# Optimization experiments

Measured on AMD Instinct MI355X. Metric: run time of the kernel, lower is better.

Reference implementation:

```python
import jax, jax.numpy as jnp
import numpy as np

N, TI, TO1 = 8, 200, 51
V, E, H, J, L = 1024, 512, 512, 512, 3
ENC_D = 512


def setup_inputs() -> dict:
    key = jax.random.key(0)
    ks = jax.random.split(key, 11)
    s = lambda k, shape, sc: jax.random.normal(k, shape, jnp.float32) * sc
    return {
        "enc_out": s(ks[0], (N, TI, ENC_D), 1.0),
        "tgt_pad": jax.random.randint(ks[1], (N, TO1), 0, V),
        "embed": s(ks[2], (V, E), 0.02),          # nn.Embedding weight
        "w_ih": s(ks[3], (L, 4 * H, E), 0.04),    # LSTM input-hidden (gate order i,f,g,o)
        "w_hh": s(ks[4], (L, 4 * H, H), 0.04),    # LSTM hidden-hidden
        "b_ih": s(ks[5], (L, 4 * H), 0.04),
        "b_hh": s(ks[6], (L, 4 * H), 0.04),
        "enc_w": s(ks[7], (J, ENC_D), 0.04),      # enc_proj (no bias)
        "dec_w": s(ks[8], (J, H), 0.04),          # dec_proj weight
        "dec_b": s(ks[9], (J,), 0.04),            # dec_proj bias
        "out_w": s(ks[10], (V, J), 0.04),         # output (no bias)
    }


def lstm_layer(x, wih, whh, bih, bhh):
    # x: [N, T, E] -> [N, T, H]; PyTorch LSTM gate order i, f, g, o
    n = x.shape[0]
    h0 = jnp.zeros((n, whh.shape[1]), x.dtype)
    c0 = jnp.zeros_like(h0)
    gin = jnp.einsum('nte,ge->ntg', x, wih) + bih + bhh  # precompute input contributions

    def step(carry, g_t):
        h, c = carry
        g = g_t + h @ whh.T
        i, f, gg, o = jnp.split(g, 4, axis=-1)
        c = jax.nn.sigmoid(f) * c + jax.nn.sigmoid(i) * jnp.tanh(gg)
        h = jax.nn.sigmoid(o) * jnp.tanh(c)
        return (h, c), h

    _, hs = jax.lax.scan(step, (h0, c0), jnp.swapaxes(gin, 0, 1))
    return jnp.swapaxes(hs, 0, 1)


def reference(enc_out, tgt_pad, embed, w_ih, w_hh, b_ih, b_hh, enc_w, dec_w, dec_b, out_w):
    # embedding lookup
    x = embed[tgt_pad]                                   # [N, To+1, E]
    # 3-layer unidirectional LSTM
    for l in range(w_ih.shape[0]):
        x = lstm_layer(x, w_ih[l], w_hh[l], b_ih[l], b_hh[l])
    # projections
    enc_p = jnp.einsum('ntd,jd->ntj', enc_out, enc_w)    # [N, Ti, J]
    dec_p = jnp.einsum('nud,jd->nuj', x, dec_w) + dec_b  # [N, To+1, J]
    # joint: broadcast add -> tanh -> output linear (no bias)
    add = enc_p[:, :, None, :] + dec_p[:, None, :, :]    # [N, Ti, To+1, J]
    return jnp.einsum('ntuj,vj->ntuv', jnp.tanh(add), out_w)  # [N, Ti, To+1, V]
```

## Files before the change

### kernel.cpp

```cpp
#include <hip/hip_runtime.h>
#include <cstdint>
#include <cstddef>

typedef __attribute__((ext_vector_type(4))) float f32x4;
typedef __attribute__((ext_vector_type(8))) short bf16x8;
typedef __attribute__((ext_vector_type(8))) unsigned short u16x8;
typedef __attribute__((ext_vector_type(4))) float float4v;
typedef __attribute__((ext_vector_type(2))) unsigned long long u64x2;
typedef unsigned long long ull;

#define NB   8
#define TIN  200
#define TO1  51
#define VSZ  1024
#define HSZ  512
static constexpr int MJOINT = NB * TIN * TO1;
static constexpr int MROWS  = TO1 * NB;

static constexpr size_t B_ENCBF = 0;
static constexpr size_t B_ENCW  = B_ENCBF + 1664ull*512*2;
static constexpr size_t B_DECW  = B_ENCW  + 512ull*512*2;
static constexpr size_t B_OUTW  = B_DECW  + 512ull*512*2;
static constexpr size_t B_WIH   = B_OUTW  + 1024ull*512*2;
static constexpr size_t B_WHH   = B_WIH   + 3ull*2048*512*2;
static constexpr size_t B_XTR   = B_WHH   + 3ull*2048*512*2;
static constexpr size_t B_BSUM  = B_XTR   + 4ull*408*512*2;
static constexpr size_t B_FLAGS = B_BSUM  + 3ull*2048*4;
static constexpr size_t B_ENCP  = B_FLAGS + 8192;
static constexpr size_t B_DECP  = B_ENCP  + 1664ull*512*4;
static constexpr size_t B_ABUF  = B_DECP  + 512ull*512*4;

__device__ __forceinline__ unsigned short f2bf(float f) {
  union { float f; unsigned u; } v; v.f = f;
  unsigned r = v.u + 0x7FFFu + ((v.u >> 16) & 1u);
  return (unsigned short)(r >> 16);
}
__device__ __forceinline__ float fast_tanh(float x) {
  float t = __expf(2.0f * x);
  return 1.0f - 2.0f / (t + 1.0f);
}
__device__ __forceinline__ float fast_sig(float x) {
  return 1.0f / (1.0f + __expf(-x));
}
__device__ __forceinline__ void gll16(const void* g, void* l) {
  __builtin_amdgcn_global_load_lds(
      (const __attribute__((address_space(1))) unsigned int*)g,
      (__attribute__((address_space(3))) unsigned int*)l, 16, 0, 0);
}
__device__ __forceinline__ void cvt8(const float* s, unsigned short* d) {
  const float4v* sp = (const float4v*)s;
  float4v x = sp[0], y = sp[1];
  u16x8 o;
  o[0]=f2bf(x[0]); o[1]=f2bf(x[1]); o[2]=f2bf(x[2]); o[3]=f2bf(x[3]);
  o[4]=f2bf(y[0]); o[5]=f2bf(y[1]); o[6]=f2bf(y[2]); o[7]=f2bf(y[3]);
  *(u16x8*)d = o;
}

static constexpr int N_ENC  = 102400;
static constexpr int N_ENCW = 32768;
static constexpr int N_DECW = 32768;
static constexpr int N_OUTW = 65536;
static constexpr int N_WIH  = 393216;
static constexpr int P0 = N_ENC, P1 = P0+N_ENCW, P2 = P1+N_DECW, P3 = P2+N_OUTW,
                     P4 = P3+N_WIH;

__global__ __launch_bounds__(256) void cvt_all(const float* __restrict__ enc,
                                               const float* __restrict__ encw,
                                               const float* __restrict__ decw,
                                               const float* __restrict__ outw,
                                               const float* __restrict__ wih,
                                               const float* __restrict__ whh,
                                               unsigned short* __restrict__ d_enc,
                                               unsigned short* __restrict__ d_encw,
                                               unsigned short* __restrict__ d_decw,
                                               unsigned short* __restrict__ d_outw,
                                               unsigned short* __restrict__ d_wih,
                                               unsigned short* __restrict__ d_whh) {
  int i = blockIdx.x * 256 + threadIdx.x;
  const float* s; unsigned short* d; int rel;
  if      (i < P0) { s = enc;  d = d_enc;  rel = i; }
  else if (i < P1) { s = encw; d = d_encw; rel = i - P0; }
  else if (i < P2) { s = decw; d = d_decw; rel = i - P1; }
  else if (i < P3) { s = outw; d = d_outw; rel = i - P2; }
  else if (i < P4) { s = wih;  d = d_wih;  rel = i - P3; }
  else             { s = whh;  d = d_whh;  rel = i - P4; }
  cvt8(s + (size_t)rel * 8, d + (size_t)rel * 8);
}

__global__ __launch_bounds__(256) void bsum_kernel(const float* __restrict__ a,
                                                   const float* __restrict__ b,
                                                   float* __restrict__ o, int n) {
  int i = blockIdx.x * 256 + threadIdx.x;
  if (i < n) o[i] = a[i] + b[i];
}

__global__ __launch_bounds__(256) void embed_kernel(const float* __restrict__ emb,
                                                    const int* __restrict__ tgt,
                                                    unsigned short* __restrict__ x0) {
  int idx = blockIdx.x * 256 + threadIdx.x;
  if (idx >= MROWS * 64) return;
  int m = idx >> 6, kc = (idx & 63) * 8;
  int t = m >> 3, n = m & 7;
  int v = tgt[n * TO1 + t];
  cvt8(emb + (size_t)v * 512 + kc, x0 + (size_t)m * 512 + kc);
}

__global__ __launch_bounds__(256) void gemm_bf16(const unsigned short* __restrict__ A,
                                                 const unsigned short* __restrict__ B,
                                                 float* __restrict__ C,
                                                 const float* __restrict__ bias,
                                                 int M, int N, int K) {
  __shared__ __align__(16) unsigned short lds[2][2][4096];
  const int tid = threadIdx.x;
  const int wave = tid >> 6, lane = tid & 63;
  const int lr = lane & 15, lg = lane >> 4;
  const int wm = (wave >> 1) * 64, wn = (wave & 1) * 64;
  const int xsl = (lg ^ (lr & 3)) << 3;

  const int nwg = gridDim.x * gridDim.y;
  const int id = blockIdx.y * gridDim.x + blockIdx.x;
  const int q = nwg >> 3, r = nwg & 7, xcd = id & 7, rest = id >> 3;
  const int nid = (xcd < r ? xcd * (q + 1) : r * (q + 1) + (xcd - r) * q) + rest;
  const size_t n0 = (size_t)(nid % gridDim.x) * 128;
  const size_t m0 = (size_t)(nid / gridDim.x) * 128;

  f32x4 acc[4][4];
#pragma unroll
  for (int i = 0; i < 4; ++i)
#pragma unroll
    for (int j = 0; j < 4; ++j) acc[i][j] = (f32x4){0.f, 0.f, 0.f, 0.f};

#define STAGE(bf, kt)                                                                 \
  do {                                                                                \
    _Pragma("unroll") for (int u = 0; u < 2; ++u) {                                   \
      const int s = u * 256 + tid;                                                    \
      const int row_ = s >> 2;                                                        \
      const int ch = (s & 3) ^ (row_ & 3);                                            \
      gll16(A + (m0 + row_) * (size_t)K + (kt) + ch * 8,                              \
            &lds[bf][0][(u * 256 + wave * 64) * 8]);                                  \
    }                                                                                 \
    _Pragma("unroll") for (int u = 0; u < 2; ++u) {                                   \
      const int s = u * 256 + tid;                                                    \
      const int row_ = s >> 2;                                                        \
      const int ch = (s & 3) ^ (row_ & 3);                                            \
      gll16(B + (n0 + row_) * (size_t)K + (kt) + ch * 8,                              \
            &lds[bf][1][(u * 256 + wave * 64) * 8]);                                  \
    }                                                                                 \
  } while (0)

  const int nt = K >> 5;
  int cur = 0;
  STAGE(0, 0);
  for (int t = 0; t < nt; ++t) {
    if (t + 1 < nt) {
      STAGE(cur ^ 1, (t + 1) * 32);
      asm volatile("s_waitcnt vmcnt(4)" ::: "memory");
    } else {
      asm volatile("s_waitcnt vmcnt(0)" ::: "memory");
    }
    __builtin_amdgcn_s_barrier();
    const unsigned short* As_ = lds[cur][0];
    const unsigned short* Bs_ = lds[cur][1];
    bf16x8 a[4], b[4];
#pragma unroll
    for (int i = 0; i < 4; ++i) a[i] = *(const bf16x8*)&As_[(wm + i * 16 + lr) * 32 + xsl];
#pragma unroll
    for (int j = 0; j < 4; ++j) b[j] = *(const bf16x8*)&Bs_[(wn + j * 16 + lr) * 32 + xsl];
    __builtin_amdgcn_s_setprio(1);
#pragma unroll
    for (int i = 0; i < 4; ++i)
#pragma unroll
      for (int j = 0; j < 4; ++j)
        acc[i][j] = __builtin_amdgcn_mfma_f32_16x16x32_bf16(a[i], b[j], acc[i][j], 0, 0, 0);
    __builtin_amdgcn_s_setprio(0);
    __builtin_amdgcn_s_barrier();
    cur ^= 1;
  }
#undef STAGE

  const int rq = lg * 4;
#pragma unroll
  for (int j = 0; j < 4; ++j) {
    const int col = (int)n0 + wn + j * 16 + lr;
    const float bv = bias ? bias[col] : 0.0f;
#pragma unroll
    for (int i = 0; i < 4; ++i) {
#pragma unroll
      for (int q2 = 0; q2 < 4; ++q2) {
        const long m = (long)m0 + wm + i * 16 + rq + q2;
        if (m < M) C[(size_t)m * N + col] = acc[i][j][q2] + bv;
      }
    }
  }
}

__global__ __launch_bounds__(512, 2) void gemm256(const unsigned short* __restrict__ A,
                                                  const unsigned short* __restrict__ B,
                                                  float* __restrict__ C,
                                                  int M, int N, int K) {
  __shared__ __align__(16) unsigned short lds[2][2][16384];
  const int tid = threadIdx.x;
  const int wave = tid >> 6, lane = tid & 63;
  const int lr = lane & 15, lg = lane >> 4;
  const int wr = (wave >> 2) * 128;
  const int wc = (wave & 3) * 64;

  const int nwg = gridDim.x * gridDim.y;
  const int id = blockIdx.y * gridDim.x + blockIdx.x;
  const int q = nwg >> 3, r = nwg & 7, xcd = id & 7, rest = id >> 3;
  const int nid = (xcd < r ? xcd * (q + 1) : r * (q + 1) + (xcd - r) * q) + rest;
  const size_t n0 = (size_t)(nid % gridDim.x) * 256;
  const size_t m0 = (size_t)(nid / gridDim.x) * 256;

  f32x4 acc[8][4];
#pragma unroll
  for (int i = 0; i < 8; ++i)
#pragma unroll
    for (int j = 0; j < 4; ++j) acc[i][j] = (f32x4){0.f, 0.f, 0.f, 0.f};

#define STG(bf, kt)                                                                    \
  do {                                                                                 \
    _Pragma("unroll") for (int u = 0; u < 4; ++u) {                                    \
      const int idx = u * 512 + tid;                                                   \
      const int row_ = idx >> 3;                                                       \
      const int ch = (idx & 7) ^ (row_ & 7);                                           \
      gll16(A + (m0 + row_) * (size_t)K + (kt) + ch * 8,                               \
            &lds[bf][0][(u * 512 + wave * 64) * 8]);                                   \
    }                                                                                  \
    _Pragma("unroll") for (int u = 0; u < 4; ++u) {                                    \
      const int idx = u * 512 + tid;                                                   \
      const int row_ = idx >> 3;                                                       \
      const int ch = (idx & 7) ^ (row_ & 7);                                           \
      gll16(B + (n0 + row_) * (size_t)K + (kt) + ch * 8,                               \
            &lds[bf][1][(u * 512 + wave * 64) * 8]);                                   \
    }                                                                                  \
  } while (0)

  const int nt = K >> 6;
  int cur = 0;
  STG(0, 0);
  for (int t = 0; t < nt; ++t) {
    if (t + 1 < nt) {
      STG(cur ^ 1, (t + 1) * 64);
      asm volatile("s_waitcnt vmcnt(8)" ::: "memory");
    } else {
      asm volatile("s_waitcnt vmcnt(0)" ::: "memory");
    }
    __builtin_amdgcn_s_barrier();
    const unsigned short* As_ = lds[cur][0];
    const unsigned short* Bs_ = lds[cur][1];
    bf16x8 b[4][2];
#pragma unroll
    for (int j = 0; j < 4; ++j) {
      const int rb = wc + j * 16 + lr;
      const int sw = rb & 7;
      b[j][0] = *(const bf16x8*)&Bs_[rb * 64 + ((lg ^ sw) << 3)];
      b[j][1] = *(const bf16x8*)&Bs_[rb * 64 + (((4 + lg) ^ sw) << 3)];
    }
    __builtin_amdgcn_s_setprio(1);
#pragma unroll
    for (int i = 0; i < 8; ++i) {
      const int ra = wr + i * 16 + lr;
      const int swa = ra & 7;
      bf16x8 a0 = *(const bf16x8*)&As_[ra * 64 + ((lg ^ swa) << 3)];
      bf16x8 a1 = *(const bf16x8*)&As_[ra * 64 + (((4 + lg) ^ swa) << 3)];
#pragma unroll
      for (int j = 0; j < 4; ++j) {
        acc[i][j] = __builtin_amdgcn_mfma_f32_16x16x32_bf16(a0, b[j][0], acc[i][j], 0, 0, 0);
        acc[i][j] = __builtin_amdgcn_mfma_f32_16x16x32_bf16(a1, b[j][1], acc[i][j], 0, 0, 0);
      }
    }
    __builtin_amdgcn_s_setprio(0);
    __builtin_amdgcn_s_barrier();
    cur ^= 1;
  }
#undef STG

#pragma unroll
  for (int i = 0; i < 8; ++i) {
#pragma unroll
    for (int q2 = 0; q2 < 4; ++q2) {
      const long m = (long)m0 + wr + i * 16 + lg * 4 + q2;
      if (m < M) {
        float* crow = C + (size_t)m * N + n0 + wc;
#pragma unroll
        for (int j = 0; j < 4; ++j) crow[j * 16 + lr] = acc[i][j][q2];
      }
    }
  }
}

__global__ __launch_bounds__(256) void rnn_kernel(const unsigned short* __restrict__ wih,
                                                  const unsigned short* __restrict__ whh,
                                                  const float* __restrict__ bsum,
                                                  unsigned short* __restrict__ xtr,
                                                  int* __restrict__ flags) {
  __shared__ __align__(16) unsigned short w_s[64 * 1024];
  __shared__ __align__(16) unsigned short x_s[8 * 512];
  __shared__ __align__(16) unsigned short h_s[8 * 512];
  __shared__ float gates_s[4][8][16];

  const int tid = threadIdx.x;
  const int l = blockIdx.x >> 5;
  const int b32 = blockIdx.x & 31;
  const int hid0 = b32 << 4;
  const int wave = tid >> 6, lane = tid & 63;
  const int lr = lane & 15, lg = lane >> 4;
  const int r7 = lr & 7;
  const int rw = wave * 16 + lr;

  {
    const int rl = tid >> 2;
    const int qt = tid & 3;
    const size_t R = (size_t)l * 2048 + (size_t)(rl >> 4) * 512 + hid0 + (rl & 15);
    const unsigned short* s0 = wih + R * 512;
    const unsigned short* s1 = whh + R * 512;
#pragma unroll
    for (int i = 0; i < 32; ++i) {
      int c = qt * 32 + i;
      bf16x8 wv = (c < 64) ? *(const bf16x8*)&s0[c * 8] : *(const bf16x8*)&s1[(c - 64) * 8];
      *(bf16x8*)&w_s[rl * 1024 + ((c ^ (rl & 7)) << 3)] = wv;
    }
  }
  const float bias = bsum[(size_t)l * 2048 + (size_t)wave * 512 + hid0 + lr];

  const unsigned short* xin = xtr + (size_t)l * MROWS * 512;
  unsigned short* xout = xtr + (size_t)(l + 1) * MROWS * 512;
  float c_reg = 0.f;
  const int srow = tid >> 5;
  const int sc = tid & 31;
  __syncthreads();

#define STAGE_TILE(SRC_ROW0, BUF)                                                      \
  do {                                                                                 \
    const ull* p_ = (const ull*)((SRC_ROW0) + (size_t)srow * 512);                     \
    _Pragma("unroll") for (int k_ = 0; k_ < 2; ++k_) {                                 \
      const int c_ = sc + k_ * 32;                                                     \
      ull v0_ = __hip_atomic_load(p_ + c_ * 2,     __ATOMIC_RELAXED, __HIP_MEMORY_SCOPE_AGENT); \
      ull v1_ = __hip_atomic_load(p_ + c_ * 2 + 1, __ATOMIC_RELAXED, __HIP_MEMORY_SCOPE_AGENT); \
      *(u64x2*)&(BUF)[srow * 512 + ((c_ ^ srow) << 3)] = (u64x2){v0_, v1_};            \
    }                                                                                  \
  } while (0)

#define POLL(FIDX_EXPR, NEED)                                                          \
  do {                                                                                 \
    if (wave == 0) {                                                                   \
      for (;;) {                                                                       \
        bool ok_ = true;                                                               \
        if (lane < 32)                                                                 \
          ok_ = __hip_atomic_load(&flags[(FIDX_EXPR) * 16], __ATOMIC_RELAXED,          \
                                  __HIP_MEMORY_SCOPE_AGENT) >= (NEED);                 \
        if (__all(ok_)) break;                                                         \
        __builtin_amdgcn_s_sleep(1);                                                   \
      }                                                                                \
    }                                                                                  \
  } while (0)

  f32x4 ax0, ax1;

  if (l > 0) POLL((l - 1) * 32 + lane, 1);
  __syncthreads();
  STAGE_TILE(xin, x_s);
  __syncthreads();
  ax0 = (f32x4){0.f, 0.f, 0.f, 0.f};
  ax1 = (f32x4){0.f, 0.f, 0.f, 0.f};
#pragma unroll
  for (int c16 = 0; c16 < 16; ++c16) {
    const int cc = c16 * 4 + lg;
    bf16x8 av = *(const bf16x8*)&x_s[r7 * 512 + ((cc ^ r7) << 3)];
    bf16x8 bv = *(const bf16x8*)&w_s[rw * 1024 + ((cc ^ r7) << 3)];
    if (c16 & 1) ax1 = __builtin_amdgcn_mfma_f32_16x16x32_bf16(av, bv, ax1, 0, 0, 0);
    else         ax0 = __builtin_amdgcn_mfma_f32_16x16x32_bf16(av, bv, ax0, 0, 0, 0);
  }

  for (int t = 0; t < TO1; ++t) {
    f32x4 acc0 = ax0, acc1 = ax1;
    if (t > 0) {
      POLL(l * 32 + lane, t);
      __syncthreads();
      STAGE_TILE(xout + (size_t)(t - 1) * 8 * 512, h_s);
      __syncthreads();
#pragma unroll
      for (int c16 = 0; c16 < 16; ++c16) {
        const int cc = c16 * 4 + lg;
        bf16x8 av = *(const bf16x8*)&h_s[r7 * 512 + ((cc ^ r7) << 3)];
        bf16x8 bv = *(const bf16x8*)&w_s[rw * 1024 + (((64 + cc) ^ r7) << 3)];
        if (c16 & 1) acc1 = __builtin_amdgcn_mfma_f32_16x16x32_bf16(av, bv, acc1, 0, 0, 0);
        else         acc0 = __builtin_amdgcn_mfma_f32_16x16x32_bf16(av, bv, acc0, 0, 0, 0);
      }
    }

    {
      f32x4 g = acc0 + acc1;
      const int nb4 = lg * 4;
#pragma unroll
      for (int q2 = 0; q2 < 4; ++q2) {
        int n = nb4 + q2;
        if (n < 8) gates_s[wave][n][lr] = g[q2] + bias;
      }
    }
    __syncthreads();
    if (tid < 128) {
      const int n = tid >> 4, j = tid & 15;
      float gi = gates_s[0][n][j], gf = gates_s[1][n][j];
      float gg = gates_s[2][n][j], go = gates_s[3][n][j];
      c_reg = fast_sig(gf) * c_reg + fast_sig(gi) * fast_tanh(gg);
      float ht = fast_sig(go) * fast_tanh(c_reg);
      float htn = __shfl_down(ht, 1);
      if (!(j & 1)) {
        unsigned pk = (unsigned)f2bf(ht) | ((unsigned)f2bf(htn) << 16);
        unsigned* dst = (unsigned*)(xout + ((size_t)t * 8 + n) * 512 + hid0 + j);
        __hip_atomic_store(dst, pk, __ATOMIC_RELAXED, __HIP_MEMORY_SCOPE_AGENT);
      }
    }
    asm volatile("s_waitcnt vmcnt(0)" ::: "memory");
    __syncthreads();
    if (tid == 0)
      __hip_atomic_store(&flags[(l * 32 + b32) * 16], t + 1,
                         __ATOMIC_RELAXED, __HIP_MEMORY_SCOPE_AGENT);

    if (t + 1 < TO1) {
      if (l > 0) POLL((l - 1) * 32 + lane, t + 2);
      __syncthreads();
      STAGE_TILE(xin + (size_t)(t + 1) * 8 * 512, x_s);
      __syncthreads();
      ax0 = (f32x4){0.f, 0.f, 0.f, 0.f};
      ax1 = (f32x4){0.f, 0.f, 0.f, 0.f};
#pragma unroll
      for (int c16 = 0; c16 < 16; ++c16) {
        const int cc = c16 * 4 + lg;
        bf16x8 av = *(const bf16x8*)&x_s[r7 * 512 + ((cc ^ r7) << 3)];
        bf16x8 bv = *(const bf16x8*)&w_s[rw * 1024 + ((cc ^ r7) << 3)];
        if (c16 & 1) ax1 = __builtin_amdgcn_mfma_f32_16x16x32_bf16(av, bv, ax1, 0, 0, 0);
        else         ax0 = __builtin_amdgcn_mfma_f32_16x16x32_bf16(av, bv, ax0, 0, 0, 0);
      }
    }
  }
#undef STAGE_TILE
#undef POLL
}

__global__ __launch_bounds__(256) void tanha_kernel(const float* __restrict__ encp,
                                                    const float* __restrict__ decp,
                                                    unsigned short* __restrict__ Ab) {
  size_t idx = (size_t)blockIdx.x * 256 + threadIdx.x;
  int m = (int)(idx >> 6);
  int kc = ((int)idx & 63) * 8;
  if (m >= 81664) return;
  u16x8 o;
  if (m >= MJOINT) {
    o[0]=0;o[1]=0;o[2]=0;o[3]=0;o[4]=0;o[5]=0;o[6]=0;o[7]=0;
  } else {
    int n = m / (TIN * TO1);
    int rem = m - n * (TIN * TO1);
    int t = rem / TO1;
    int u = rem - t * TO1;
    const float4v* ep = (const float4v*)(encp + ((size_t)n * TIN + t) * 512 + kc);
    const float4v* dp = (const float4v*)(decp + ((size_t)u * 8 + n) * 512 + kc);
    float4v e0 = ep[0], e1 = ep[1], d0 = dp[0], d1 = dp[1];
    o[0]=f2bf(fast_tanh(e0[0]+d0[0])); o[1]=f2bf(fast_tanh(e0[1]+d0[1]));
    o[2]=f2bf(fast_tanh(e0[2]+d0[2])); o[3]=f2bf(fast_tanh(e0[3]+d0[3]));
    o[4]=f2bf(fast_tanh(e1[0]+d1[0])); o[5]=f2bf(fast_tanh(e1[1]+d1[1]));
    o[6]=f2bf(fast_tanh(e1[2]+d1[2])); o[7]=f2bf(fast_tanh(e1[3]+d1[3]));
  }
  *(u16x8*)(Ab + (size_t)m * 512 + kc) = o;
}

extern "C" void kernel_launch(void* const* d_in, const int* in_sizes, int n_in,
                              void* d_out, int out_size, void* d_ws, size_t ws_size,
                              hipStream_t stream) {
  (void)in_sizes; (void)n_in; (void)out_size; (void)ws_size;
  const float* enc_out = (const float*)d_in[0];
  const int*   tgt     = (const int*)d_in[1];
  const float* embed   = (const float*)d_in[2];
  const float* w_ih    = (const float*)d_in[3];
  const float* w_hh    = (const float*)d_in[4];
  const float* b_ih    = (const float*)d_in[5];
  const float* b_hh    = (const float*)d_in[6];
  const float* enc_w   = (const float*)d_in[7];
  const float* dec_w   = (const float*)d_in[8];
  const float* dec_b   = (const float*)d_in[9];
  const float* out_w   = (const float*)d_in[10];

  char* ws = (char*)d_ws;
  unsigned short* enc_bf  = (unsigned short*)(ws + B_ENCBF);
  unsigned short* encw_bf = (unsigned short*)(ws + B_ENCW);
  unsigned short* decw_bf = (unsigned short*)(ws + B_DECW);
  unsigned short* outw_bf = (unsigned short*)(ws + B_OUTW);
  unsigned short* wih_bf  = (unsigned short*)(ws + B_WIH);
  unsigned short* whh_bf  = (unsigned short*)(ws + B_WHH);
  unsigned short* xtr     = (unsigned short*)(ws + B_XTR);
  float* bsum  = (float*)(ws + B_BSUM);
  int*   flags = (int*)(ws + B_FLAGS);
  float* encp  = (float*)(ws + B_ENCP);
  float* decp  = (float*)(ws + B_DECP);
  unsigned short* abuf = (unsigned short*)(ws + B_ABUF);
  float* Cout  = (float*)d_out;

  hipMemsetAsync(flags, 0, 6144, stream);

  cvt_all<<<3984, 256, 0, stream>>>(enc_out, enc_w, dec_w, out_w, w_ih, w_hh,
                                    enc_bf, encw_bf, decw_bf, outw_bf, wih_bf, whh_bf);
  bsum_kernel<<<24, 256, 0, stream>>>(b_ih, b_hh, bsum, 6144);
  embed_kernel<<<102, 256, 0, stream>>>(embed, tgt, xtr);

  rnn_kernel<<<96, 256, 0, stream>>>(wih_bf, whh_bf, bsum, xtr, flags);

  gemm_bf16<<<dim3(4, 13), 256, 0, stream>>>(enc_bf, encw_bf, encp, nullptr, NB * TIN, 512, 512);
  gemm_bf16<<<dim3(4, 4), 256, 0, stream>>>(xtr + 3ull * MROWS * 512, decw_bf, decp, dec_b,
                                            MROWS, 512, 512);
  tanha_kernel<<<20416, 256, 0, stream>>>(encp, decp, abuf);
  gemm256<<<dim3(4, 319), 512, 0, stream>>>(abuf, outw_bf, Cout, MJOINT, VSZ, 512);
}
```

Baseline: 388.5 us.

## Fuse tanh joint into output GEMM A-load and overlap enc projection with RNN

The separate tanh kernel and its 81664x512 bf16 staging buffer are removed. The output GEMM now computes tanh(enc_p+dec_p) in registers and writes it into LDS as its A tile. The encoder projection GEMM runs as 52 extra blocks inside the RNN launch so it overlaps the latency-bound recurrence, and the flag memset moves into the convert kernel. In exchange, each GEMM tile recomputes tanh from fp32 loads with register staging instead of async LDS loads. The 2-waves occupancy hint is dropped, and a full vmcnt(0) wait plus syncthreads per k-step may reduce overlap.

```diff
diff --git a/kernel.cpp b/kernel.cpp
--- a/kernel.cpp
+++ b/kernel.cpp
@@ -28,7 +28,6 @@
 static constexpr size_t B_FLAGS = B_BSUM  + 3ull*2048*4;
 static constexpr size_t B_ENCP  = B_FLAGS + 8192;
 static constexpr size_t B_DECP  = B_ENCP  + 1664ull*512*4;
-static constexpr size_t B_ABUF  = B_DECP  + 512ull*512*4;
 
 __device__ __forceinline__ unsigned short f2bf(float f) {
   union { float f; unsigned u; } v; v.f = f;
@@ -75,7 +74,9 @@
                                                unsigned short* __restrict__ d_decw,
                                                unsigned short* __restrict__ d_outw,
                                                unsigned short* __restrict__ d_wih,
-                                               unsigned short* __restrict__ d_whh) {
+                                               unsigned short* __restrict__ d_whh,
+                                               int* __restrict__ flags) {
+  if (blockIdx.x == 0 && threadIdx.x < 96) flags[threadIdx.x * 16] = 0;
   int i = blockIdx.x * 256 + threadIdx.x;
   const float* s; unsigned short* d; int rel;
   if      (i < P0) { s = enc;  d = d_enc;  rel = i; }
@@ -194,10 +195,10 @@
   }
 }
 
-__global__ __launch_bounds__(512, 2) void gemm256(const unsigned short* __restrict__ A,
-                                                  const unsigned short* __restrict__ B,
-                                                  float* __restrict__ C,
-                                                  int M, int N, int K) {
+__global__ __launch_bounds__(512) void gemm256f(const float* __restrict__ encp,
+                                                const float* __restrict__ decp,
+                                                const unsigned short* __restrict__ B,
+                                                float* __restrict__ C) {
   __shared__ __align__(16) unsigned short lds[2][2][16384];
   const int tid = threadIdx.x;
   const int wave = tid >> 6, lane = tid & 63;
@@ -212,41 +213,72 @@
   const size_t n0 = (size_t)(nid % gridDim.x) * 256;
   const size_t m0 = (size_t)(nid / gridDim.x) * 256;
 
+  const int arow = tid >> 1;
+  const int ahalf = tid & 1;
+  int n_, t_, u_;
+  {
+    long m = (long)m0 + arow;
+    if (m >= MJOINT) { n_ = 0; t_ = 0; u_ = 0; }
+    else {
+      n_ = (int)(m / (TIN * TO1));
+      int rem = (int)(m - (long)n_ * (TIN * TO1));
+      t_ = rem / TO1;
+      u_ = rem - t_ * TO1;
+    }
+  }
+  const float* ep = encp + ((size_t)n_ * TIN + t_) * 512 + ahalf * 32;
+  const float* dp = decp + ((size_t)u_ * 8 + n_) * 512 + ahalf * 32;
+
   f32x4 acc[8][4];
 #pragma unroll
   for (int i = 0; i < 8; ++i)
 #pragma unroll
     for (int j = 0; j < 4; ++j) acc[i][j] = (f32x4){0.f, 0.f, 0.f, 0.f};
 
-#define STG(bf, kt)                                                                    \
+  float4v ea[8], da[8];
+#define AISSUE(kt)                                                                     \
   do {                                                                                 \
-    _Pragma("unroll") for (int u = 0; u < 4; ++u) {                                    \
-      const int idx = u * 512 + tid;                                                   \
+    _Pragma("unroll") for (int i_ = 0; i_ < 8; ++i_) {                                 \
+      ea[i_] = *(const float4v*)(ep + (kt) + i_ * 4);                                  \
+      da[i_] = *(const float4v*)(dp + (kt) + i_ * 4);                                  \
+    }                                                                                  \
+  } while (0)
+#define AWRITE(bf)                                                                     \
+  do {                                                                                 \
+    _Pragma("unroll") for (int i_ = 0; i_ < 4; ++i_) {                                 \
+      u16x8 o_;                                                                        \
+      _Pragma("unroll") for (int j_ = 0; j_ < 4; ++j_) {                               \
+        o_[j_]     = f2bf(fast_tanh(ea[2 * i_][j_]     + da[2 * i_][j_]));             \
+        o_[4 + j_] = f2bf(fast_tanh(ea[2 * i_ + 1][j_] + da[2 * i_ + 1][j_]));         \
+      }                                                                                \
+      const int sl_ = (ahalf * 4 + i_) ^ (arow & 7);                                   \
+      *(u16x8*)&lds[bf][0][arow * 64 + sl_ * 8] = o_;                                  \
+    }                                                                                  \
+  } while (0)
+#define BSTG(bf, kt)                                                                   \
+  do {                                                                                 \
+    _Pragma("unroll") for (int u2 = 0; u2 < 4; ++u2) {                                 \
+      const int idx = u2 * 512 + tid;                                                  \
       const int row_ = idx >> 3;                                                       \
       const int ch = (idx & 7) ^ (row_ & 7);                                           \
-      gll16(A + (m0 + row_) * (size_t)K + (kt) + ch * 8,                               \
-            &lds[bf][0][(u * 512 + wave * 64) * 8]);                                   \
-    }                                                                                  \
-    _Pragma("unroll") for (int u = 0; u < 4; ++u) {                                    \
-      const int idx = u * 512 + tid;                                                   \
-      const int row_ = idx >> 3;                                                       \
-      const int ch = (idx & 7) ^ (row_ & 7);                                           \
-      gll16(B + (n0 + row_) * (size_t)K + (kt) + ch * 8,                               \
-            &lds[bf][1][(u * 512 + wave * 64) * 8]);                                   \
+      gll16(B + (n0 + row_) * (size_t)512 + (kt) + ch * 8,                             \
+            &lds[bf][1][(u2 * 512 + wave * 64) * 8]);                                  \
     }                                                                                  \
   } while (0)
 
-  const int nt = K >> 6;
   int cur = 0;
-  STG(0, 0);
-  for (int t = 0; t < nt; ++t) {
-    if (t + 1 < nt) {
-      STG(cur ^ 1, (t + 1) * 64);
-      asm volatile("s_waitcnt vmcnt(8)" ::: "memory");
-    } else {
-      asm volatile("s_waitcnt vmcnt(0)" ::: "memory");
-    }
-    __builtin_amdgcn_s_barrier();
+  AISSUE(0);
+  BSTG(0, 0);
+  asm volatile("s_waitcnt vmcnt(0)" ::: "memory");
+  AWRITE(0);
+  __syncthreads();
+
+  for (int t = 0; t < 8; ++t) {
+    const int nxt = cur ^ 1;
+    if (t < 7) {
+      AISSUE((t + 1) * 64);
+      BSTG(nxt, (t + 1) * 64);
+    }
     const unsigned short* As_ = lds[cur][0];
     const unsigned short* Bs_ = lds[cur][1];
     bf16x8 b[4][2];
@@ -271,18 +303,24 @@
       }
     }
     __builtin_amdgcn_s_setprio(0);
-    __builtin_amdgcn_s_barrier();
-    cur ^= 1;
-  }
-#undef STG
+    if (t < 7) {
+      asm volatile("s_waitcnt vmcnt(0)" ::: "memory");
+      AWRITE(nxt);
+    }
+    __syncthreads();
+    cur = nxt;
+  }
+#undef AISSUE
+#undef AWRITE
+#undef BSTG
 
 #pragma unroll
   for (int i = 0; i < 8; ++i) {
 #pragma unroll
     for (int q2 = 0; q2 < 4; ++q2) {
       const long m = (long)m0 + wr + i * 16 + lg * 4 + q2;
-      if (m < M) {
-        float* crow = C + (size_t)m * N + n0 + wc;
+      if (m < MJOINT) {
+        float* crow = C + (size_t)m * VSZ + n0 + wc;
 #pragma unroll
         for (int j = 0; j < 4; ++j) crow[j * 16 + lr] = acc[i][j][q2];
       }
@@ -290,22 +328,106 @@
   }
 }
 
-__global__ __launch_bounds__(256) void rnn_kernel(const unsigned short* __restrict__ wih,
-                                                  const unsigned short* __restrict__ whh,
-                                                  const float* __restrict__ bsum,
-                                                  unsigned short* __restrict__ xtr,
-                                                  int* __restrict__ flags) {
+__global__ __launch_bounds__(256) void rnn_enc_kernel(const unsigned short* __restrict__ wih,
+                                                      const unsigned short* __restrict__ whh,
+                                                      const float* __restrict__ bsum,
+                                                      unsigned short* __restrict__ xtr,
+                                                      int* __restrict__ flags,
+                                                      const unsigned short* __restrict__ eA,
+                                                      const unsigned short* __restrict__ eB,
+                                                      float* __restrict__ eC) {
   __shared__ __align__(16) unsigned short w_s[64 * 1024];
   __shared__ __align__(16) unsigned short x_s[8 * 512];
   __shared__ __align__(16) unsigned short h_s[8 * 512];
   __shared__ float gates_s[4][8][16];
 
   const int tid = threadIdx.x;
+  const int wave = tid >> 6, lane = tid & 63;
+  const int lr = lane & 15, lg = lane >> 4;
+
+  if (blockIdx.x >= 96) {
+    unsigned short* eld = w_s;
+    const int g = blockIdx.x - 96;
+    const int wm = (wave >> 1) * 64, wn = (wave & 1) * 64;
+    const int xsl = (lg ^ (lr & 3)) << 3;
+    const int nwg = 52;
+    const int q = nwg >> 3, r = nwg & 7, xcd = g & 7, rest = g >> 3;
+    const int nid = (xcd < r ? xcd * (q + 1) : r * (q + 1) + (xcd - r) * q) + rest;
+    const size_t n0 = (size_t)(nid & 3) * 128;
+    const size_t m0 = (size_t)(nid >> 2) * 128;
+
+    f32x4 acc[4][4];
+#pragma unroll
+    for (int i = 0; i < 4; ++i)
+#pragma unroll
+      for (int j = 0; j < 4; ++j) acc[i][j] = (f32x4){0.f, 0.f, 0.f, 0.f};
+
+#define ESTG(bf, kt)                                                                   \
+    do {                                                                               \
+      _Pragma("unroll") for (int u = 0; u < 2; ++u) {                                  \
+        const int s = u * 256 + tid;                                                   \
+        const int row_ = s >> 2;                                                       \
+        const int ch = (s & 3) ^ (row_ & 3);                                           \
+        gll16(eA + (m0 + row_) * 512 + (kt) + ch * 8,                                  \
+              &eld[(bf) * 8192 + (u * 256 + wave * 64) * 8]);                          \
+      }                                                                                \
+      _Pragma("unroll") for (int u = 0; u < 2; ++u) {                                  \
+        const int s = u * 256 + tid;                                                   \
+        const int row_ = s >> 2;                                                       \
+        const int ch = (s & 3) ^ (row_ & 3);                                           \
+        gll16(eB + (n0 + row_) * 512 + (kt) + ch * 8,                                  \
+              &eld[(bf) * 8192 + 4096 + (u * 256 + wave * 64) * 8]);                   \
+      }                                                                                \
+    } while (0)
+
+    int cur = 0;
+    ESTG(0, 0);
+    for (int t = 0; t < 16; ++t) {
+      if (t + 1 < 16) {
+        ESTG(cur ^ 1, (t + 1) * 32);
+        asm volatile("s_waitcnt vmcnt(4)" ::: "memory");
+      } else {
+        asm volatile("s_waitcnt vmcnt(0)" ::: "memory");
+      }
+      __builtin_amdgcn_s_barrier();
+      const unsigned short* As_ = eld + cur * 8192;
+      const unsigned short* Bs_ = As_ + 4096;
+      bf16x8 a[4], b[4];
+#pragma unroll
+      for (int i = 0; i < 4; ++i) a[i] = *(const bf16x8*)&As_[(wm + i * 16 + lr) * 32 + xsl];
+#pragma unroll
+      for (int j = 0; j < 4; ++j) b[j] = *(const bf16x8*)&Bs_[(wn + j * 16 + lr) * 32 + xsl];
+      __builtin_amdgcn_s_setprio(1);
+#pragma unroll
+      for (int i = 0; i < 4; ++i)
+#pragma unroll
+        for (int j = 0; j < 4; ++j)
+          acc[i][j] = __builtin_amdgcn_mfma_f32_16x16x32_bf16(a[i], b[j], acc[i][j], 0, 0, 0);
+      __builtin_amdgcn_s_setprio(0);
+      __builtin_amdgcn_s_barrier();
+      cur ^= 1;
+    }
+#undef ESTG
+
+    const int rq = lg * 4;
+#pragma unroll
+    for (int j = 0; j < 4; ++j) {
+      const int col = (int)n0 + wn + j * 16 + lr;
+#pragma unroll
+      for (int i = 0; i < 4; ++i) {
+#pragma unroll
+        for (int q2 = 0; q2 < 4; ++q2) {
+          const long m = (long)m0 + wm + i * 16 + rq + q2;
+          eC[(size_t)m * 512 + col] = acc[i][j][q2];
+        }
+      }
+    }
+    return;
+  }
+
   const int l = blockIdx.x >> 5;
   const int b32 = blockIdx.x & 31;
   const int hid0 = b32 << 4;
-  const int wave = tid >> 6, lane = tid & 63;
-  const int lr = lane & 15, lg = lane >> 4;
   const int r7 = lr & 7;
   const int rw = wave * 16 + lr;
 
@@ -438,32 +560,6 @@
   }
 #undef STAGE_TILE
 #undef POLL
-}
-
-__global__ __launch_bounds__(256) void tanha_kernel(const float* __restrict__ encp,
-                                                    const float* __restrict__ decp,
-                                                    unsigned short* __restrict__ Ab) {
-  size_t idx = (size_t)blockIdx.x * 256 + threadIdx.x;
-  int m = (int)(idx >> 6);
-  int kc = ((int)idx & 63) * 8;
-  if (m >= 81664) return;
-  u16x8 o;
-  if (m >= MJOINT) {
-    o[0]=0;o[1]=0;o[2]=0;o[3]=0;o[4]=0;o[5]=0;o[6]=0;o[7]=0;
-  } else {
-    int n = m / (TIN * TO1);
-    int rem = m - n * (TIN * TO1);
-    int t = rem / TO1;
-    int u = rem - t * TO1;
-    const float4v* ep = (const float4v*)(encp + ((size_t)n * TIN + t) * 512 + kc);
-    const float4v* dp = (const float4v*)(decp + ((size_t)u * 8 + n) * 512 + kc);
-    float4v e0 = ep[0], e1 = ep[1], d0 = dp[0], d1 = dp[1];
-    o[0]=f2bf(fast_tanh(e0[0]+d0[0])); o[1]=f2bf(fast_tanh(e0[1]+d0[1]));
-    o[2]=f2bf(fast_tanh(e0[2]+d0[2])); o[3]=f2bf(fast_tanh(e0[3]+d0[3]));
-    o[4]=f2bf(fast_tanh(e1[0]+d1[0])); o[5]=f2bf(fast_tanh(e1[1]+d1[1]));
-    o[6]=f2bf(fast_tanh(e1[2]+d1[2])); o[7]=f2bf(fast_tanh(e1[3]+d1[3]));
-  }
-  *(u16x8*)(Ab + (size_t)m * 512 + kc) = o;
 }
 
 extern "C" void kernel_launch(void* const* d_in, const int* in_sizes, int n_in,
@@ -494,21 +590,18 @@
   int*   flags = (int*)(ws + B_FLAGS);
   float* encp  = (float*)(ws + B_ENCP);
   float* decp  = (float*)(ws + B_DECP);
-  unsigned short* abuf = (unsigned short*)(ws + B_ABUF);
   float* Cout  = (float*)d_out;
 
-  hipMemsetAsync(flags, 0, 6144, stream);
-
   cvt_all<<<3984, 256, 0, stream>>>(enc_out, enc_w, dec_w, out_w, w_ih, w_hh,
-                                    enc_bf, encw_bf, decw_bf, outw_bf, wih_bf, whh_bf);
+                                    enc_bf, encw_bf, decw_bf, outw_bf, wih_bf, whh_bf,
+                                    flags);
   bsum_kernel<<<24, 256, 0, stream>>>(b_ih, b_hh, bsum, 6144);
   embed_kernel<<<102, 256, 0, stream>>>(embed, tgt, xtr);
 
-  rnn_kernel<<<96, 256, 0, stream>>>(wih_bf, whh_bf, bsum, xtr, flags);
-
-  gemm_bf16<<<dim3(4, 13), 256, 0, stream>>>(enc_bf, encw_bf, encp, nullptr, NB * TIN, 512, 512);
+  rnn_enc_kernel<<<148, 256, 0, stream>>>(wih_bf, whh_bf, bsum, xtr, flags,
+                                          enc_bf, encw_bf, encp);
+
   gemm_bf16<<<dim3(4, 4), 256, 0, stream>>>(xtr + 3ull * MROWS * 512, decw_bf, decp, dec_b,
                                             MROWS, 512, 512);
-  tanha_kernel<<<20416, 256, 0, stream>>>(encp, decp, abuf);
-  gemm256<<<dim3(4, 319), 512, 0, stream>>>(abuf, outw_bf, Cout, MJOINT, VSZ, 512);
-}
+  gemm256f<<<dim3(4, 319), 512, 0, stream>>>(encp, decp, outw_bf, Cout);
+}
```

Measured after the change: 449.0 us. 15.6% more time.

## Co-schedule encoder projection GEMM with the LSTM recurrence in one launch

Applied to the files above, without the earlier changes.

The encoder projection GEMM is merged into the persistent LSTM kernel as 52 extra blocks, so it runs on otherwise idle CUs while the 96 recurrence blocks work through their serial time steps. The flag reset moves from a separate memset into the conversion kernel, which removes one launch. The risk is that the GEMM blocks compete with the latency-bound recurrence blocks for scheduling or memory bandwidth. It also relies on all 148 blocks being resident at once so the flag polling does not deadlock.

```diff
diff --git a/kernel.cpp b/kernel.cpp
--- a/kernel.cpp
+++ b/kernel.cpp
@@ -75,7 +75,9 @@
                                                unsigned short* __restrict__ d_decw,
                                                unsigned short* __restrict__ d_outw,
                                                unsigned short* __restrict__ d_wih,
-                                               unsigned short* __restrict__ d_whh) {
+                                               unsigned short* __restrict__ d_whh,
+                                               int* __restrict__ flags) {
+  if (blockIdx.x == 0 && threadIdx.x < 96) flags[threadIdx.x * 16] = 0;
   int i = blockIdx.x * 256 + threadIdx.x;
   const float* s; unsigned short* d; int rel;
   if      (i < P0) { s = enc;  d = d_enc;  rel = i; }
@@ -288,156 +290,6 @@
       }
     }
   }
-}
-
-__global__ __launch_bounds__(256) void rnn_kernel(const unsigned short* __restrict__ wih,
-                                                  const unsigned short* __restrict__ whh,
-                                                  const float* __restrict__ bsum,
-                                                  unsigned short* __restrict__ xtr,
-                                                  int* __restrict__ flags) {
-  __shared__ __align__(16) unsigned short w_s[64 * 1024];
-  __shared__ __align__(16) unsigned short x_s[8 * 512];
-  __shared__ __align__(16) unsigned short h_s[8 * 512];
-  __shared__ float gates_s[4][8][16];
-
-  const int tid = threadIdx.x;
-  const int l = blockIdx.x >> 5;
-  const int b32 = blockIdx.x & 31;
-  const int hid0 = b32 << 4;
-  const int wave = tid >> 6, lane = tid & 63;
-  const int lr = lane & 15, lg = lane >> 4;
-  const int r7 = lr & 7;
-  const int rw = wave * 16 + lr;
-
-  {
-    const int rl = tid >> 2;
-    const int qt = tid & 3;
-    const size_t R = (size_t)l * 2048 + (size_t)(rl >> 4) * 512 + hid0 + (rl & 15);
-    const unsigned short* s0 = wih + R * 512;
-    const unsigned short* s1 = whh + R * 512;
-#pragma unroll
-    for (int i = 0; i < 32; ++i) {
-      int c = qt * 32 + i;
-      bf16x8 wv = (c < 64) ? *(const bf16x8*)&s0[c * 8] : *(const bf16x8*)&s1[(c - 64) * 8];
-      *(bf16x8*)&w_s[rl * 1024 + ((c ^ (rl & 7)) << 3)] = wv;
-    }
-  }
-  const float bias = bsum[(size_t)l * 2048 + (size_t)wave * 512 + hid0 + lr];
-
-  const unsigned short* xin = xtr + (size_t)l * MROWS * 512;
-  unsigned short* xout = xtr + (size_t)(l + 1) * MROWS * 512;
-  float c_reg = 0.f;
-  const int srow = tid >> 5;
-  const int sc = tid & 31;
-  __syncthreads();
-
-#define STAGE_TILE(SRC_ROW0, BUF)                                                      \
-  do {                                                                                 \
-    const ull* p_ = (const ull*)((SRC_ROW0) + (size_t)srow * 512);                     \
-    _Pragma("unroll") for (int k_ = 0; k_ < 2; ++k_) {                                 \
-      const int c_ = sc + k_ * 32;                                                     \
-      ull v0_ = __hip_atomic_load(p_ + c_ * 2,     __ATOMIC_RELAXED, __HIP_MEMORY_SCOPE_AGENT); \
-      ull v1_ = __hip_atomic_load(p_ + c_ * 2 + 1, __ATOMIC_RELAXED, __HIP_MEMORY_SCOPE_AGENT); \
-      *(u64x2*)&(BUF)[srow * 512 + ((c_ ^ srow) << 3)] = (u64x2){v0_, v1_};            \
-    }                                                                                  \
-  } while (0)
-
-#define POLL(FIDX_EXPR, NEED)                                                          \
-  do {                                                                                 \
-    if (wave == 0) {                                                                   \
-      for (;;) {                                                                       \
-        bool ok_ = true;                                                               \
-        if (lane < 32)                                                                 \
-          ok_ = __hip_atomic_load(&flags[(FIDX_EXPR) * 16], __ATOMIC_RELAXED,          \
-                                  __HIP_MEMORY_SCOPE_AGENT) >= (NEED);                 \
-        if (__all(ok_)) break;                                                         \
-        __builtin_amdgcn_s_sleep(1);                                                   \
-      }                                                                                \
-    }                                                                                  \
-  } while (0)
-
-  f32x4 ax0, ax1;
-
-  if (l > 0) POLL((l - 1) * 32 + lane, 1);
-  __syncthreads();
-  STAGE_TILE(xin, x_s);
-  __syncthreads();
-  ax0 = (f32x4){0.f, 0.f, 0.f, 0.f};
-  ax1 = (f32x4){0.f, 0.f, 0.f, 0.f};
-#pragma unroll
-  for (int c16 = 0; c16 < 16; ++c16) {
-    const int cc = c16 * 4 + lg;
-    bf16x8 av = *(const bf16x8*)&x_s[r7 * 512 + ((cc ^ r7) << 3)];
-    bf16x8 bv = *(const bf16x8*)&w_s[rw * 1024 + ((cc ^ r7) << 3)];
-    if (c16 & 1) ax1 = __builtin_amdgcn_mfma_f32_16x16x32_bf16(av, bv, ax1, 0, 0, 0);
-    else         ax0 = __builtin_amdgcn_mfma_f32_16x16x32_bf16(av, bv, ax0, 0, 0, 0);
-  }
-
-  for (int t = 0; t < TO1; ++t) {
-    f32x4 acc0 = ax0, acc1 = ax1;
-    if (t > 0) {
-      POLL(l * 32 + lane, t);
-      __syncthreads();
-      STAGE_TILE(xout + (size_t)(t - 1) * 8 * 512, h_s);
-      __syncthreads();
-#pragma unroll
-      for (int c16 = 0; c16 < 16; ++c16) {
-        const int cc = c16 * 4 + lg;
-        bf16x8 av = *(const bf16x8*)&h_s[r7 * 512 + ((cc ^ r7) << 3)];
-        bf16x8 bv = *(const bf16x8*)&w_s[rw * 1024 + (((64 + cc) ^ r7) << 3)];
-        if (c16 & 1) acc1 = __builtin_amdgcn_mfma_f32_16x16x32_bf16(av, bv, acc1, 0, 0, 0);
-        else         acc0 = __builtin_amdgcn_mfma_f32_16x16x32_bf16(av, bv, acc0, 0, 0, 0);
-      }
-    }
-
-    {
-      f32x4 g = acc0 + acc1;
-      const int nb4 = lg * 4;
-#pragma unroll
-      for (int q2 = 0; q2 < 4; ++q2) {
-        int n = nb4 + q2;
-        if (n < 8) gates_s[wave][n][lr] = g[q2] + bias;
-      }
-    }
-    __syncthreads();
-    if (tid < 128) {
-      const int n = tid >> 4, j = tid & 15;
-      float gi = gates_s[0][n][j], gf = gates_s[1][n][j];
-      float gg = gates_s[2][n][j], go = gates_s[3][n][j];
-      c_reg = fast_sig(gf) * c_reg + fast_sig(gi) * fast_tanh(gg);
-      float ht = fast_sig(go) * fast_tanh(c_reg);
-      float htn = __shfl_down(ht, 1);
-      if (!(j & 1)) {
-        unsigned pk = (unsigned)f2bf(ht) | ((unsigned)f2bf(htn) << 16);
-        unsigned* dst = (unsigned*)(xout + ((size_t)t * 8 + n) * 512 + hid0 + j);
-        __hip_atomic_store(dst, pk, __ATOMIC_RELAXED, __HIP_MEMORY_SCOPE_AGENT);
-      }
-    }
-    asm volatile("s_waitcnt vmcnt(0)" ::: "memory");
-    __syncthreads();
-    if (tid == 0)
-      __hip_atomic_store(&flags[(l * 32 + b32) * 16], t + 1,
-                         __ATOMIC_RELAXED, __HIP_MEMORY_SCOPE_AGENT);
-
-    if (t + 1 < TO1) {
-      if (l > 0) POLL((l - 1) * 32 + lane, t + 2);
-      __syncthreads();
-      STAGE_TILE(xin + (size_t)(t + 1) * 8 * 512, x_s);
-      __syncthreads();
-      ax0 = (f32x4){0.f, 0.f, 0.f, 0.f};
-      ax1 = (f32x4){0.f, 0.f, 0.f, 0.f};
-#pragma unroll
-      for (int c16 = 0; c16 < 16; ++c16) {
-        const int cc = c16 * 4 + lg;
-        bf16x8 av = *(const bf16x8*)&x_s[r7 * 512 + ((cc ^ r7) << 3)];
-        bf16x8 bv = *(const bf16x8*)&w_s[rw * 1024 + ((cc ^ r7) << 3)];
-        if (c16 & 1) ax1 = __builtin_amdgcn_mfma_f32_16x16x32_bf16(av, bv, ax1, 0, 0, 0);
-        else         ax0 = __builtin_amdgcn_mfma_f32_16x16x32_bf16(av, bv, ax0, 0, 0, 0);
-      }
-    }
-  }
-#undef STAGE_TILE
-#undef POLL
 }
 
 __global__ __launch_bounds__(256) void tanha_kernel(const float* __restrict__ encp,
@@ -466,6 +318,240 @@
   *(u16x8*)(Ab + (size_t)m * 512 + kc) = o;
 }
 
+__global__ __launch_bounds__(256) void rnn_enc_kernel(const unsigned short* __restrict__ wih,
+                                                      const unsigned short* __restrict__ whh,
+                                                      const float* __restrict__ bsum,
+                                                      unsigned short* __restrict__ xtr,
+                                                      int* __restrict__ flags,
+                                                      const unsigned short* __restrict__ eA,
+                                                      const unsigned short* __restrict__ eB,
+                                                      float* __restrict__ eC) {
+  __shared__ __align__(16) unsigned short w_s[64 * 1024];
+  __shared__ __align__(16) unsigned short x_s[8 * 512];
+  __shared__ __align__(16) unsigned short h_s[8 * 512];
+  __shared__ float gates_s[4][8][16];
+
+  const int tid = threadIdx.x;
+  const int wave = tid >> 6, lane = tid & 63;
+  const int lr = lane & 15, lg = lane >> 4;
+
+  if (blockIdx.x >= 96) {
+    unsigned short* eld = w_s;
+    const int g = blockIdx.x - 96;
+    const int wm = (wave >> 1) * 64, wn = (wave & 1) * 64;
+    const int xsl = (lg ^ (lr & 3)) << 3;
+    const int nwg = 52;
+    const int q = nwg >> 3, r = nwg & 7, xcd = g & 7, rest = g >> 3;
+    const int nid = (xcd < r ? xcd * (q + 1) : r * (q + 1) + (xcd - r) * q) + rest;
+    const size_t n0 = (size_t)(nid & 3) * 128;
+    const size_t m0 = (size_t)(nid >> 2) * 128;
+
+    f32x4 acc[4][4];
+#pragma unroll
+    for (int i = 0; i < 4; ++i)
+#pragma unroll
+      for (int j = 0; j < 4; ++j) acc[i][j] = (f32x4){0.f, 0.f, 0.f, 0.f};
+
+#define ESTG(bf, kt)                                                                   \
+    do {                                                                               \
+      _Pragma("unroll") for (int u = 0; u < 2; ++u) {                                  \
+        const int s = u * 256 + tid;                                                   \
+        const int row_ = s >> 2;                                                       \
+        const int ch = (s & 3) ^ (row_ & 3);                                           \
+        gll16(eA + (m0 + row_) * 512 + (kt) + ch * 8,                                  \
+              &eld[(bf) * 8192 + (u * 256 + wave * 64) * 8]);                          \
+      }                                                                                \
+      _Pragma("unroll") for (int u = 0; u < 2; ++u) {                                  \
+        const int s = u * 256 + tid;                                                   \
+        const int row_ = s >> 2;                                                       \
+        const int ch = (s & 3) ^ (row_ & 3);                                           \
+        gll16(eB + (n0 + row_) * 512 + (kt) + ch * 8,                                  \
+              &eld[(bf) * 8192 + 4096 + (u * 256 + wave * 64) * 8]);                   \
+      }                                                                                \
+    } while (0)
+
+    int cur = 0;
+    ESTG(0, 0);
+    for (int t = 0; t < 16; ++t) {
+      if (t + 1 < 16) {
+        ESTG(cur ^ 1, (t + 1) * 32);
+        asm volatile("s_waitcnt vmcnt(4)" ::: "memory");
+      } else {
+        asm volatile("s_waitcnt vmcnt(0)" ::: "memory");
+      }
+      __builtin_amdgcn_s_barrier();
+      const unsigned short* As_ = eld + cur * 8192;
+      const unsigned short* Bs_ = As_ + 4096;
+      bf16x8 a[4], b[4];
+#pragma unroll
+      for (int i = 0; i < 4; ++i) a[i] = *(const bf16x8*)&As_[(wm + i * 16 + lr) * 32 + xsl];
+#pragma unroll
+      for (int j = 0; j < 4; ++j) b[j] = *(const bf16x8*)&Bs_[(wn + j * 16 + lr) * 32 + xsl];
+      __builtin_amdgcn_s_setprio(1);
+#pragma unroll
+      for (int i = 0; i < 4; ++i)
+#pragma unroll
+        for (int j = 0; j < 4; ++j)
+          acc[i][j] = __builtin_amdgcn_mfma_f32_16x16x32_bf16(a[i], b[j], acc[i][j], 0, 0, 0);
+      __builtin_amdgcn_s_setprio(0);
+      __builtin_amdgcn_s_barrier();
+      cur ^= 1;
+    }
+#undef ESTG
+
+    const int rq = lg * 4;
+#pragma unroll
+    for (int j = 0; j < 4; ++j) {
+      const int col = (int)n0 + wn + j * 16 + lr;
+#pragma unroll
+      for (int i = 0; i < 4; ++i) {
+#pragma unroll
+        for (int q2 = 0; q2 < 4; ++q2) {
+          const long m = (long)m0 + wm + i * 16 + rq + q2;
+          eC[(size_t)m * 512 + col] = acc[i][j][q2];
+        }
+      }
+    }
+    return;
+  }
+
+  const int l = blockIdx.x >> 5;
+  const int b32 = blockIdx.x & 31;
+  const int hid0 = b32 << 4;
+  const int r7 = lr & 7;
+  const int rw = wave * 16 + lr;
+
+  {
+    const int rl = tid >> 2;
+    const int qt = tid & 3;
+    const size_t R = (size_t)l * 2048 + (size_t)(rl >> 4) * 512 + hid0 + (rl & 15);
+    const unsigned short* s0 = wih + R * 512;
+    const unsigned short* s1 = whh + R * 512;
+#pragma unroll
+    for (int i = 0; i < 32; ++i) {
+      int c = qt * 32 + i;
+      bf16x8 wv = (c < 64) ? *(const bf16x8*)&s0[c * 8] : *(const bf16x8*)&s1[(c - 64) * 8];
+      *(bf16x8*)&w_s[rl * 1024 + ((c ^ (rl & 7)) << 3)] = wv;
+    }
+  }
+  const float bias = bsum[(size_t)l * 2048 + (size_t)wave * 512 + hid0 + lr];
+
+  const unsigned short* xin = xtr + (size_t)l * MROWS * 512;
+  unsigned short* xout = xtr + (size_t)(l + 1) * MROWS * 512;
+  float c_reg = 0.f;
+  const int srow = tid >> 5;
+  const int sc = tid & 31;
+  __syncthreads();
+
+#define STAGE_TILE(SRC_ROW0, BUF)                                                      \
+  do {                                                                                 \
+    const ull* p_ = (const ull*)((SRC_ROW0) + (size_t)srow * 512);                     \
+    _Pragma("unroll") for (int k_ = 0; k_ < 2; ++k_) {                                 \
+      const int c_ = sc + k_ * 32;                                                     \
+      ull v0_ = __hip_atomic_load(p_ + c_ * 2,     __ATOMIC_RELAXED, __HIP_MEMORY_SCOPE_AGENT); \
+      ull v1_ = __hip_atomic_load(p_ + c_ * 2 + 1, __ATOMIC_RELAXED, __HIP_MEMORY_SCOPE_AGENT); \
+      *(u64x2*)&(BUF)[srow * 512 + ((c_ ^ srow) << 3)] = (u64x2){v0_, v1_};            \
+    }                                                                                  \
+  } while (0)
+
+#define POLL(FIDX_EXPR, NEED)                                                          \
+  do {                                                                                 \
+    if (wave == 0) {                                                                   \
+      for (;;) {                                                                       \
+        bool ok_ = true;                                                               \
+        if (lane < 32)                                                                 \
+          ok_ = __hip_atomic_load(&flags[(FIDX_EXPR) * 16], __ATOMIC_RELAXED,          \
+                                  __HIP_MEMORY_SCOPE_AGENT) >= (NEED);                 \
+        if (__all(ok_)) break;                                                         \
+        __builtin_amdgcn_s_sleep(1);                                                   \
+      }                                                                                \
+    }                                                                                  \
+  } while (0)
+
+  f32x4 ax0, ax1;
+
+  if (l > 0) POLL((l - 1) * 32 + lane, 1);
+  __syncthreads();
+  STAGE_TILE(xin, x_s);
+  __syncthreads();
+  ax0 = (f32x4){0.f, 0.f, 0.f, 0.f};
+  ax1 = (f32x4){0.f, 0.f, 0.f, 0.f};
+#pragma unroll
+  for (int c16 = 0; c16 < 16; ++c16) {
+    const int cc = c16 * 4 + lg;
+    bf16x8 av = *(const bf16x8*)&x_s[r7 * 512 + ((cc ^ r7) << 3)];
+    bf16x8 bv = *(const bf16x8*)&w_s[rw * 1024 + ((cc ^ r7) << 3)];
+    if (c16 & 1) ax1 = __builtin_amdgcn_mfma_f32_16x16x32_bf16(av, bv, ax1, 0, 0, 0);
+    else         ax0 = __builtin_amdgcn_mfma_f32_16x16x32_bf16(av, bv, ax0, 0, 0, 0);
+  }
+
+  for (int t = 0; t < TO1; ++t) {
+    f32x4 acc0 = ax0, acc1 = ax1;
+    if (t > 0) {
+      POLL(l * 32 + lane, t);
+      __syncthreads();
+      STAGE_TILE(xout + (size_t)(t - 1) * 8 * 512, h_s);
+      __syncthreads();
+#pragma unroll
+      for (int c16 = 0; c16 < 16; ++c16) {
+        const int cc = c16 * 4 + lg;
+        bf16x8 av = *(const bf16x8*)&h_s[r7 * 512 + ((cc ^ r7) << 3)];
+        bf16x8 bv = *(const bf16x8*)&w_s[rw * 1024 + (((64 + cc) ^ r7) << 3)];
+        if (c16 & 1) acc1 = __builtin_amdgcn_mfma_f32_16x16x32_bf16(av, bv, acc1, 0, 0, 0);
+        else         acc0 = __builtin_amdgcn_mfma_f32_16x16x32_bf16(av, bv, acc0, 0, 0, 0);
+      }
+    }
+
+    {
+      f32x4 g = acc0 + acc1;
+      const int nb4 = lg * 4;
+#pragma unroll
+      for (int q2 = 0; q2 < 4; ++q2) {
+        int n = nb4 + q2;
+        if (n < 8) gates_s[wave][n][lr] = g[q2] + bias;
+      }
+    }
+    __syncthreads();
+    if (tid < 128) {
+      const int n = tid >> 4, j = tid & 15;
+      float gi = gates_s[0][n][j], gf = gates_s[1][n][j];
+      float gg = gates_s[2][n][j], go = gates_s[3][n][j];
+      c_reg = fast_sig(gf) * c_reg + fast_sig(gi) * fast_tanh(gg);
+      float ht = fast_sig(go) * fast_tanh(c_reg);
+      float htn = __shfl_down(ht, 1);
+      if (!(j & 1)) {
+        unsigned pk = (unsigned)f2bf(ht) | ((unsigned)f2bf(htn) << 16);
+        unsigned* dst = (unsigned*)(xout + ((size_t)t * 8 + n) * 512 + hid0 + j);
+        __hip_atomic_store(dst, pk, __ATOMIC_RELAXED, __HIP_MEMORY_SCOPE_AGENT);
+      }
+    }
+    asm volatile("s_waitcnt vmcnt(0)" ::: "memory");
+    __syncthreads();
+    if (tid == 0)
+      __hip_atomic_store(&flags[(l * 32 + b32) * 16], t + 1,
+                         __ATOMIC_RELAXED, __HIP_MEMORY_SCOPE_AGENT);
+
+    if (t + 1 < TO1) {
+      if (l > 0) POLL((l - 1) * 32 + lane, t + 2);
+      __syncthreads();
+      STAGE_TILE(xin + (size_t)(t + 1) * 8 * 512, x_s);
+      __syncthreads();
+      ax0 = (f32x4){0.f, 0.f, 0.f, 0.f};
+      ax1 = (f32x4){0.f, 0.f, 0.f, 0.f};
+#pragma unroll
+      for (int c16 = 0; c16 < 16; ++c16) {
+        const int cc = c16 * 4 + lg;
+        bf16x8 av = *(const bf16x8*)&x_s[r7 * 512 + ((cc ^ r7) << 3)];
+        bf16x8 bv = *(const bf16x8*)&w_s[rw * 1024 + ((cc ^ r7) << 3)];
+        if (c16 & 1) ax1 = __builtin_amdgcn_mfma_f32_16x16x32_bf16(av, bv, ax1, 0, 0, 0);
+        else         ax0 = __builtin_amdgcn_mfma_f32_16x16x32_bf16(av, bv, ax0, 0, 0, 0);
+      }
+    }
+  }
+#undef STAGE_TILE
+#undef POLL
+}
+
 extern "C" void kernel_launch(void* const* d_in, const int* in_sizes, int n_in,
                               void* d_out, int out_size, void* d_ws, size_t ws_size,
                               hipStream_t stream) {
@@ -497,16 +583,15 @@
   unsigned short* abuf = (unsigned short*)(ws + B_ABUF);
   float* Cout  = (float*)d_out;
 
-  hipMemsetAsync(flags, 0, 6144, stream);
-
   cvt_all<<<3984, 256, 0, stream>>>(enc_out, enc_w, dec_w, out_w, w_ih, w_hh,
-                                    enc_bf, encw_bf, decw_bf, outw_bf, wih_bf, whh_bf);
+                                    enc_bf, encw_bf, decw_bf, outw_bf, wih_bf, whh_bf,
+                                    flags);
   bsum_kernel<<<24, 256, 0, stream>>>(b_ih, b_hh, bsum, 6144);
   embed_kernel<<<102, 256, 0, stream>>>(embed, tgt, xtr);
 
-  rnn_kernel<<<96, 256, 0, stream>>>(wih_bf, whh_bf, bsum, xtr, flags);
-
-  gemm_bf16<<<dim3(4, 13), 256, 0, stream>>>(enc_bf, encw_bf, encp, nullptr, NB * TIN, 512, 512);
+  rnn_enc_kernel<<<148, 256, 0, stream>>>(wih_bf, whh_bf, bsum, xtr, flags,
+                                          enc_bf, encw_bf, encp);
+
   gemm_bf16<<<dim3(4, 4), 256, 0, stream>>>(xtr + 3ull * MROWS * 512, decw_bf, decp, dec_b,
                                             MROWS, 512, 512);
   tanha_kernel<<<20416, 256, 0, stream>>>(encp, decp, abuf);
```

Result: faster. 368.4 us (-5.2%).
